# Kernel optimization log

Measured on AMD Instinct MI355X. Metric: run time of the kernel, lower is better.

The kernel has to match this reference:

```python
import jax, jax.numpy as jnp
import numpy as np
import math

DIM = 256

def setup_inputs() -> dict:
    key = jax.random.key(0)
    kx, kq, kk, kv = jax.random.split(key, 4)
    B, N, D = 2, 8192, DIM
    x = jax.random.normal(kx, (B, N, D), dtype=jnp.float32)
    s = 1.0 / math.sqrt(D)  # ~ PyTorch Linear init scale
    Wq = jax.random.uniform(kq, (D, D), dtype=jnp.float32, minval=-s, maxval=s)
    Wk = jax.random.uniform(kk, (D, D), dtype=jnp.float32, minval=-s, maxval=s)
    Wv = jax.random.uniform(kv, (D, D), dtype=jnp.float32, minval=-s, maxval=s)
    return {"x": x, "Wq": Wq, "Wk": Wk, "Wv": Wv}

def reference(x, Wq, Wk, Wv):
    # x: [B, N, D]; torch Linear computes x @ W.T
    Q = jnp.einsum('bnd,ed->bne', x, Wq)
    K = jnp.einsum('bnd,ed->bne', x, Wk)
    V = jnp.einsum('bnd,ed->bne', x, Wv)
    D = x.shape[-1]
    scores = jnp.einsum('bqd,bkd->bqk', Q, K) / jnp.sqrt(jnp.float32(D))
    # NOTE: softmax over dim=1 (the query axis), matching the original code
    attn = jax.nn.softmax(scores, axis=1)  # [B, N, N]
    out = jnp.einsum('bqk,bkd->bqd', attn, V)
    return out
```

## Files before the change

### kernel.cpp

```cpp
#include <hip/hip_runtime.h>
#include <hip/hip_bf16.h>


#define N_ 8192
#define SCALE 0.0625f

typedef __attribute__((ext_vector_type(8))) short short8;
typedef __attribute__((ext_vector_type(4))) float f32x4;
typedef __attribute__((ext_vector_type(4))) unsigned short ushort4_t;

__device__ inline unsigned short f2bf(float f) {
    unsigned int x = __float_as_uint(f);
    unsigned int r = (x + 0x7fffu + ((x >> 16) & 1u)) >> 16;
    return (unsigned short)r;
}

__device__ inline short8 ldg8(const unsigned short* p) {
    return *reinterpret_cast<const short8*>(p);
}

__device__ inline short8 cvt8(const float* p) {
    float4 a = *(const float4*)p;
    float4 b = *(const float4*)(p + 4);
    short8 r;
    r[0] = (short)f2bf(a.x); r[1] = (short)f2bf(a.y);
    r[2] = (short)f2bf(a.z); r[3] = (short)f2bf(a.w);
    r[4] = (short)f2bf(b.x); r[5] = (short)f2bf(b.y);
    r[6] = (short)f2bf(b.z); r[7] = (short)f2bf(b.w);
    return r;
}

__device__ inline f32x4 mfma16(short8 a, short8 b, f32x4 c) {
    return __builtin_amdgcn_mfma_f32_16x16x32_bf16(a, b, c, 0, 0, 0);
}

__device__ inline float bf2f(unsigned short u) {
    return __uint_as_float(((unsigned)u) << 16);
}

#define PIN8(v) asm volatile("" : "+v"(v))

typedef __attribute__((address_space(3))) unsigned int lds_u32;
typedef __attribute__((address_space(1))) const unsigned int glb_u32;
__device__ __forceinline__ void gll16(const void* g, void* l) {
    __builtin_amdgcn_global_load_lds((glb_u32*)g, (lds_u32*)l, 16, 0, 0);
}
#define WAIT_VM0()   asm volatile("s_waitcnt vmcnt(0)" ::: "memory")
#define WAIT_LGKM0() asm volatile("s_waitcnt lgkmcnt(0)" ::: "memory")
#define BARRIER()    __builtin_amdgcn_s_barrier()

__global__ __launch_bounds__(256) void k_cvtw(
    const float* __restrict__ Wq, const float* __restrict__ Wk,
    const float* __restrict__ Wv, unsigned short* __restrict__ Wb)
{
    int t = blockIdx.x * 256 + threadIdx.x;
    int e8 = t * 8;
    const float* src = (e8 < 65536) ? Wq + e8
                     : (e8 < 131072) ? Wk + (e8 - 65536)
                                     : Wv + (e8 - 131072);
    *reinterpret_cast<short8*>(Wb + e8) = cvt8(src);
}

__global__ __launch_bounds__(512, 1) void k_proj(
    const float* __restrict__ x, const unsigned short* __restrict__ Wb,
    unsigned short* __restrict__ Qb, unsigned short* __restrict__ Kb,
    unsigned short* __restrict__ Vt)
{
    extern __shared__ char smem[];
    unsigned short* sX = (unsigned short*)smem;
    char* sW = smem + 32768;
    const int rb = blockIdx.x;
    const int tid = threadIdx.x, w = tid >> 6, lane = tid & 63;
    const int lr = lane & 15, lg = lane >> 4;
    const int wqs = w >> 2, wes = w & 3;

    int eoff[4], doff[4];
#pragma unroll
    for (int i = 0; i < 4; ++i) {
        int L = tid + i * 512;
        int r = L >> 5, c = (L & 31) ^ (r & 7);
        eoff[i] = r * 256 + c * 8;
        doff[i] = L * 16;
    }

    const unsigned short* wsrc = Wb;
#pragma unroll
    for (int i = 0; i < 4; ++i)
        gll16(wsrc + eoff[i], sW + doff[i]);

#pragma unroll
    for (int i = 0; i < 4; ++i) {
        int g = tid + i * 512;
        int r = g >> 5, c = g & 31;
        int off = (r * 512 + c * 16) ^ ((r & 7) << 4);
        *reinterpret_cast<short8*>(reinterpret_cast<char*>(sX) + off) =
            cvt8(x + (size_t)(rb * 64 + r) * 256 + c * 8);
    }
    __syncthreads();

    short8 xf[2][8];
#pragma unroll
    for (int qf = 0; qf < 2; ++qf)
#pragma unroll
        for (int ks = 0; ks < 8; ++ks) {
            int row = wqs * 32 + qf * 16 + lr;
            int off = (row * 512 + (ks * 32 + lg * 8) * 2) ^ ((row & 7) << 4);
            xf[qf][ks] = *reinterpret_cast<const short8*>(
                reinterpret_cast<const char*>(sX) + off);
            PIN8(xf[qf][ks]);
        }

    for (int c = 0; c < 12; ++c) {
        const int cur = c & 1;
        const char* sWc = sW + cur * 32768;

        WAIT_VM0();
        BARRIER();
        __builtin_amdgcn_sched_barrier(0);

        if (c + 1 < 12) {
            const unsigned short* wn = Wb + (size_t)(c + 1) * 64 * 256;
            char* nW = sW + (cur ^ 1) * 32768;
#pragma unroll
            for (int i = 0; i < 4; ++i)
                gll16(wn + eoff[i], nW + doff[i]);
        }

        f32x4 acc[2] = {};
#pragma unroll
        for (int ks = 0; ks < 8; ++ks) {
            int row = wes * 16 + lr;
            int off = (row * 512 + (ks * 32 + lg * 8) * 2) ^ ((row & 7) << 4);
            short8 wf = *reinterpret_cast<const short8*>(sWc + off);
            acc[0] = mfma16(xf[0][ks], wf, acc[0]);
            acc[1] = mfma16(xf[1][ks], wf, acc[1]);
        }

        int mat = c >> 2;
        int ecol = (c & 3) * 64 + wes * 16 + lr;
#pragma unroll
        for (int qf = 0; qf < 2; ++qf) {
            int rbase = rb * 64 + wqs * 32 + qf * 16 + lg * 4;
            if (mat < 2) {
                unsigned short* dst = (mat == 0) ? Qb : Kb;
#pragma unroll
                for (int r = 0; r < 4; ++r)
                    dst[(size_t)(rbase + r) * 256 + ecol] = f2bf(acc[qf][r]);
            } else {
                int bidx = rbase >> 13, nr = rbase & 8191;
                ushort4_t v;
#pragma unroll
                for (int r = 0; r < 4; ++r) v[r] = f2bf(acc[qf][r]);
                *reinterpret_cast<ushort4_t*>(
                    Vt + ((size_t)bidx * 256 + ecol) * 8192 + nr) = v;
            }
        }
    }
}

__global__ __launch_bounds__(512, 1) void k_zv(
    const unsigned short* __restrict__ Qb, const unsigned short* __restrict__ Kb,
    unsigned short* __restrict__ Vt)
{
    extern __shared__ char smem[];
    __shared__ float zred[8][32];
    __shared__ float zfin[64];
    const int kt = blockIdx.x, b = blockIdx.y;
    const int tid = threadIdx.x, w = tid >> 6, lane = tid & 63;
    const int lr = lane & 15, lg = lane >> 4;
    const int qs = w & 3, kh = w >> 2;

    short8 kfr[2][8];
#pragma unroll
    for (int kn = 0; kn < 2; ++kn)
#pragma unroll
        for (int ks = 0; ks < 8; ++ks) {
            kfr[kn][ks] = ldg8(
                Kb + (size_t)(b * N_ + kt * 64 + kh * 32 + kn * 16 + lr) * 256
                   + ks * 32 + lg * 8);
            PIN8(kfr[kn][ks]);
        }

    int eoff[8], doff[8];
#pragma unroll
    for (int i = 0; i < 8; ++i) {
        int L = i * 512 + w * 64 + lane;
        int r = L >> 5, c = (L & 31) ^ (r & 7);
        eoff[i] = r * 256 + c * 8;
        doff[i] = L * 16;
    }
    const unsigned short* qbase = Qb + (size_t)b * N_ * 256;

#pragma unroll
    for (int i = 0; i < 8; ++i)
        gll16(qbase + eoff[i], smem + doff[i]);

    float zs0 = 0.f, zs1 = 0.f;
    for (int it = 0; it < 64; ++it) {
        const int cur = it & 1;
        const char* sQ = smem + cur * 65536;

        WAIT_VM0();
        BARRIER();
        __builtin_amdgcn_sched_barrier(0);

        if (it + 1 < 64) {
            const unsigned short* qsrc = qbase + (size_t)(it + 1) * 128 * 256;
            char* nQ = smem + (cur ^ 1) * 65536;
#pragma unroll
            for (int i = 0; i < 8; ++i)
                gll16(qsrc + eoff[i], nQ + doff[i]);
        }

        f32x4 acc[2][2] = {};
        __builtin_amdgcn_s_setprio(1);
#pragma unroll
        for (int ks = 0; ks < 8; ++ks) {
            int coff = (ks * 32 + lg * 8) * 2;
#pragma unroll
            for (int qf = 0; qf < 2; ++qf) {
                int row = qs * 32 + qf * 16 + lr;
                int off = (row * 512 + coff) ^ ((row & 7) << 4);
                short8 qa = *reinterpret_cast<const short8*>(sQ + off);
                acc[qf][0] = mfma16(qa, kfr[0][ks], acc[qf][0]);
                acc[qf][1] = mfma16(qa, kfr[1][ks], acc[qf][1]);
            }
        }
        __builtin_amdgcn_s_setprio(0);

#pragma unroll
        for (int qf = 0; qf < 2; ++qf)
#pragma unroll
            for (int r = 0; r < 4; ++r) {
                zs0 += __expf(acc[qf][0][r] * SCALE);
                zs1 += __expf(acc[qf][1][r] * SCALE);
            }
    }

    zs0 += __shfl_xor(zs0, 16); zs0 += __shfl_xor(zs0, 32);
    zs1 += __shfl_xor(zs1, 16); zs1 += __shfl_xor(zs1, 32);
    if (lg == 0) {
        zred[w][lr]      = zs0;
        zred[w][16 + lr] = zs1;
    }
    __syncthreads();
    if (tid < 64) {
        int kh2 = tid >> 5, kc = tid & 31;
        float z = zred[kh2 * 4 + 0][kc] + zred[kh2 * 4 + 1][kc] +
                  zred[kh2 * 4 + 2][kc] + zred[kh2 * 4 + 3][kc];
        zfin[tid] = 1.0f / z;
    }
    __syncthreads();

#pragma unroll
    for (int i = 0; i < 4; ++i) {
        int G = i * 512 + tid;
        int d = G >> 3, c = G & 7;
        unsigned short* p =
            Vt + ((size_t)b * 256 + d) * 8192 + kt * 64 + c * 8;
        short8 v = *reinterpret_cast<short8*>(p);
        short8 o;
#pragma unroll
        for (int j = 0; j < 8; ++j)
            o[j] = (short)f2bf(bf2f((unsigned short)v[j]) * zfin[c * 8 + j]);
        *reinterpret_cast<short8*>(p) = o;
    }
}

__global__ __launch_bounds__(512, 1) void k_attn(
    const unsigned short* __restrict__ Qb, const unsigned short* __restrict__ Kb,
    const unsigned short* __restrict__ Vt, float* __restrict__ out)
{
    extern __shared__ char smem[];
    const int qt = blockIdx.x, b = blockIdx.y;
    const int tid = threadIdx.x, w = tid >> 6, lane = tid & 63;
    const int lr = lane & 15, lg = lane >> 4;
    const int qbase = qt * 64;
    const int wqs = w >> 2;
    const int wks = w & 3;
    const int wds = w & 3;
    const int q0 = wqs * 32;

    const unsigned short* srcK[4];
    const unsigned short* srcV[4];
#pragma unroll
    for (int i = 0; i < 4; ++i) {
        int L = w * 256 + i * 64 + lane;
        int r = L >> 5, c = (L & 31) ^ (r & 7);
        srcK[i] = Kb + (size_t)(b * N_ + r) * 256 + c * 8;
        int d = L >> 3, c2 = (L & 7) ^ (d & 7);
        srcV[i] = Vt + ((size_t)b * 256 + d) * 8192 + c2 * 8;
    }

#pragma unroll
    for (int i = 0; i < 4; ++i) {
        gll16(srcK[i], smem + (size_t)(w * 256 + i * 64) * 16);
        gll16(srcV[i], smem + 65536 + (size_t)(w * 256 + i * 64) * 16);
        srcK[i] += 64 * 256;
        srcV[i] += 64;
    }

    short8 qfr[2][8];
#pragma unroll
    for (int qf = 0; qf < 2; ++qf) {
        const unsigned short* qrow =
            Qb + (size_t)(b * N_ + qbase + q0 + qf * 16 + lr) * 256;
#pragma unroll
        for (int ks = 0; ks < 8; ++ks) {
            qfr[qf][ks] = ldg8(qrow + ks * 32 + lg * 8);
            PIN8(qfr[qf][ks]);
        }
    }

    f32x4 acco[2][4] = {};

    for (int kt = 0; kt < 128; ++kt) {
        const int cur = kt & 1;
        char* sK = smem + cur * 32768;
        char* sV = smem + 65536 + cur * 32768;
        char* sP = smem + 131072;

        WAIT_VM0();
        BARRIER();
        __builtin_amdgcn_sched_barrier(0);

        if (kt + 1 < 128) {
            char* nK = smem + (cur ^ 1) * 32768;
            char* nV = smem + 65536 + (cur ^ 1) * 32768;
#pragma unroll
            for (int i = 0; i < 4; ++i) {
                gll16(srcK[i], nK + (size_t)(w * 256 + i * 64) * 16);
                gll16(srcV[i], nV + (size_t)(w * 256 + i * 64) * 16);
                srcK[i] += 64 * 256;
                srcV[i] += 64;
            }
        }

        f32x4 sacc[2] = {};
        __builtin_amdgcn_s_setprio(1);
#pragma unroll
        for (int ks = 0; ks < 8; ++ks) {
            int krow = wks * 16 + lr;
            int coff = (ks * 32 + lg * 8) * 2;
            int off = (krow * 512 + coff) ^ ((krow & 7) << 4);
            short8 kb = *reinterpret_cast<const short8*>(sK + off);
            sacc[0] = mfma16(qfr[0][ks], kb, sacc[0]);
            sacc[1] = mfma16(qfr[1][ks], kb, sacc[1]);
        }
        __builtin_amdgcn_s_setprio(0);

#pragma unroll
        for (int qf = 0; qf < 2; ++qf)
#pragma unroll
            for (int r = 0; r < 4; ++r) {
                float p = __expf(sacc[qf][r] * SCALE);
                int q = q0 + qf * 16 + lg * 4 + r;
                int kcol = wks * 16 + lr;
                int off = (q * 128 + kcol * 2) ^ ((q & 7) << 4);
                *reinterpret_cast<unsigned short*>(sP + off) = f2bf(p);
            }

        WAIT_LGKM0();
        BARRIER();
        __builtin_amdgcn_sched_barrier(0);

        __builtin_amdgcn_s_setprio(1);
#pragma unroll
        for (int kk = 0; kk < 2; ++kk) {
            int coff = (kk * 32 + lg * 8) * 2;
            short8 pa[2];
#pragma unroll
            for (int qf = 0; qf < 2; ++qf) {
                int qq = q0 + qf * 16 + lr;
                int offa = (qq * 128 + coff) ^ ((qq & 7) << 4);
                pa[qf] = *reinterpret_cast<const short8*>(sP + offa);
            }
#pragma unroll
            for (int df = 0; df < 4; ++df) {
                int d = wds * 64 + df * 16 + lr;
                int offb = (d * 128 + coff) ^ ((d & 7) << 4);
                short8 vb = *reinterpret_cast<const short8*>(sV + offb);
                acco[0][df] = mfma16(pa[0], vb, acco[0][df]);
                acco[1][df] = mfma16(pa[1], vb, acco[1][df]);
            }
        }
        __builtin_amdgcn_s_setprio(0);
    }

#pragma unroll
    for (int qf = 0; qf < 2; ++qf)
#pragma unroll
        for (int df = 0; df < 4; ++df) {
            int d = wds * 64 + df * 16 + lr;
            int q0r = qbase + q0 + qf * 16 + lg * 4;
#pragma unroll
            for (int r = 0; r < 4; ++r)
                out[(size_t)(b * N_ + q0r + r) * 256 + d] = acco[qf][df][r];
        }
}

extern "C" void kernel_launch(void* const* d_in, const int* in_sizes, int n_in,
                              void* d_out, int out_size, void* d_ws, size_t ws_size,
                              hipStream_t stream)
{
    const float* x  = (const float*)d_in[0];
    const float* Wq = (const float*)d_in[1];
    const float* Wk = (const float*)d_in[2];
    const float* Wv = (const float*)d_in[3];

    char* ws = (char*)d_ws;
    unsigned short* Qb = (unsigned short*)(ws);
    unsigned short* Kb = (unsigned short*)(ws + 8388608);
    unsigned short* Vt = (unsigned short*)(ws + 16777216);
    unsigned short* Wb = (unsigned short*)(ws + 25165824);
    float* out = (float*)d_out;

    k_cvtw<<<dim3(96), dim3(256), 0, stream>>>(Wq, Wk, Wv, Wb);

    hipFuncSetAttribute((const void*)k_proj,
                        hipFuncAttributeMaxDynamicSharedMemorySize, 98304);
    k_proj<<<dim3(256), dim3(512), 98304, stream>>>(x, Wb, Qb, Kb, Vt);

    hipFuncSetAttribute((const void*)k_zv,
                        hipFuncAttributeMaxDynamicSharedMemorySize, 131072);
    k_zv<<<dim3(128, 2), dim3(512), 131072, stream>>>(Qb, Kb, Vt);

    hipFuncSetAttribute((const void*)k_attn,
                        hipFuncAttributeMaxDynamicSharedMemorySize, 139264);
    k_attn<<<dim3(128, 2), dim3(512), 139264, stream>>>(Qb, Kb, Vt, out);
}
```

Before: 300.8 us.

## Enlarge attention query tile to 128 and split key range across two blocks

Each attention block now covers 128 queries instead of 64, so every K/V tile loaded into shared memory serves twice as many queries. Each wave computes a 32-key by 32-query score tile and 128 output dims. To keep the grid at 256 blocks on the GPU, the key axis is split in two. The second half writes partial sums to a workspace buffer, and a new add kernel merges them into the output. This trades lower K/V traffic per query for more registers per wave, an extra fp32 partial write and read, and one more kernel launch.

```diff
diff --git a/kernel.cpp b/kernel.cpp
--- a/kernel.cpp
+++ b/kernel.cpp
@@ -269,17 +269,19 @@
 
 __global__ __launch_bounds__(512, 1) void k_attn(
     const unsigned short* __restrict__ Qb, const unsigned short* __restrict__ Kb,
-    const unsigned short* __restrict__ Vt, float* __restrict__ out)
+    const unsigned short* __restrict__ Vt, float* __restrict__ out,
+    float* __restrict__ part, int nkt)
 {
     extern __shared__ char smem[];
-    const int qt = blockIdx.x, b = blockIdx.y;
+    const int qt = blockIdx.x, kh = blockIdx.y, b = blockIdx.z;
     const int tid = threadIdx.x, w = tid >> 6, lane = tid & 63;
     const int lr = lane & 15, lg = lane >> 4;
-    const int qbase = qt * 64;
-    const int wqs = w >> 2;
-    const int wks = w & 3;
-    const int wds = w & 3;
+    const int qbase = qt * 128;
+    const int wqs = w >> 1;
+    const int wkh = w & 1;
+    const int wds = w & 1;
     const int q0 = wqs * 32;
+    const int k0 = kh * nkt * 64;
 
     const unsigned short* srcK[4];
     const unsigned short* srcV[4];
@@ -287,9 +289,9 @@
     for (int i = 0; i < 4; ++i) {
         int L = w * 256 + i * 64 + lane;
         int r = L >> 5, c = (L & 31) ^ (r & 7);
-        srcK[i] = Kb + (size_t)(b * N_ + r) * 256 + c * 8;
+        srcK[i] = Kb + (size_t)(b * N_ + k0 + r) * 256 + c * 8;
         int d = L >> 3, c2 = (L & 7) ^ (d & 7);
-        srcV[i] = Vt + ((size_t)b * 256 + d) * 8192 + c2 * 8;
+        srcV[i] = Vt + ((size_t)b * 256 + d) * 8192 + k0 + c2 * 8;
     }
 
 #pragma unroll
@@ -312,9 +314,9 @@
         }
     }
 
-    f32x4 acco[2][4] = {};
-
-    for (int kt = 0; kt < 128; ++kt) {
+    f32x4 acco[2][8] = {};
+
+    for (int kt = 0; kt < nkt; ++kt) {
         const int cur = kt & 1;
         char* sK = smem + cur * 32768;
         char* sV = smem + 65536 + cur * 32768;
@@ -324,7 +326,7 @@
         BARRIER();
         __builtin_amdgcn_sched_barrier(0);
 
-        if (kt + 1 < 128) {
+        if (kt + 1 < nkt) {
             char* nK = smem + (cur ^ 1) * 32768;
             char* nV = smem + 65536 + (cur ^ 1) * 32768;
 #pragma unroll
@@ -336,29 +338,34 @@
             }
         }
 
-        f32x4 sacc[2] = {};
+        f32x4 sacc[2][2] = {};
         __builtin_amdgcn_s_setprio(1);
 #pragma unroll
         for (int ks = 0; ks < 8; ++ks) {
-            int krow = wks * 16 + lr;
             int coff = (ks * 32 + lg * 8) * 2;
-            int off = (krow * 512 + coff) ^ ((krow & 7) << 4);
-            short8 kb = *reinterpret_cast<const short8*>(sK + off);
-            sacc[0] = mfma16(qfr[0][ks], kb, sacc[0]);
-            sacc[1] = mfma16(qfr[1][ks], kb, sacc[1]);
+#pragma unroll
+            for (int kf = 0; kf < 2; ++kf) {
+                int krow = wkh * 32 + kf * 16 + lr;
+                int off = (krow * 512 + coff) ^ ((krow & 7) << 4);
+                short8 kb = *reinterpret_cast<const short8*>(sK + off);
+                sacc[0][kf] = mfma16(qfr[0][ks], kb, sacc[0][kf]);
+                sacc[1][kf] = mfma16(qfr[1][ks], kb, sacc[1][kf]);
+            }
         }
         __builtin_amdgcn_s_setprio(0);
 
 #pragma unroll
         for (int qf = 0; qf < 2; ++qf)
 #pragma unroll
-            for (int r = 0; r < 4; ++r) {
-                float p = __expf(sacc[qf][r] * SCALE);
-                int q = q0 + qf * 16 + lg * 4 + r;
-                int kcol = wks * 16 + lr;
-                int off = (q * 128 + kcol * 2) ^ ((q & 7) << 4);
-                *reinterpret_cast<unsigned short*>(sP + off) = f2bf(p);
-            }
+            for (int kf = 0; kf < 2; ++kf)
+#pragma unroll
+                for (int r = 0; r < 4; ++r) {
+                    float p = __expf(sacc[qf][kf][r] * SCALE);
+                    int q = q0 + qf * 16 + lg * 4 + r;
+                    int kcol = wkh * 32 + kf * 16 + lr;
+                    int off = (q * 128 + kcol * 2) ^ ((q & 7) << 4);
+                    *reinterpret_cast<unsigned short*>(sP + off) = f2bf(p);
+                }
 
         WAIT_LGKM0();
         BARRIER();
@@ -376,8 +383,8 @@
                 pa[qf] = *reinterpret_cast<const short8*>(sP + offa);
             }
 #pragma unroll
-            for (int df = 0; df < 4; ++df) {
-                int d = wds * 64 + df * 16 + lr;
+            for (int df = 0; df < 8; ++df) {
+                int d = wds * 128 + df * 16 + lr;
                 int offb = (d * 128 + coff) ^ ((d & 7) << 4);
                 short8 vb = *reinterpret_cast<const short8*>(sV + offb);
                 acco[0][df] = mfma16(pa[0], vb, acco[0][df]);
@@ -387,16 +394,31 @@
         __builtin_amdgcn_s_setprio(0);
     }
 
+    float* dst = (kh == 0) ? out : part;
 #pragma unroll
     for (int qf = 0; qf < 2; ++qf)
 #pragma unroll
-        for (int df = 0; df < 4; ++df) {
-            int d = wds * 64 + df * 16 + lr;
+        for (int df = 0; df < 8; ++df) {
+            int d = wds * 128 + df * 16 + lr;
             int q0r = qbase + q0 + qf * 16 + lg * 4;
 #pragma unroll
             for (int r = 0; r < 4; ++r)
-                out[(size_t)(b * N_ + q0r + r) * 256 + d] = acco[qf][df][r];
-        }
+                dst[(size_t)(b * N_ + q0r + r) * 256 + d] = acco[qf][df][r];
+        }
+}
+
+__global__ __launch_bounds__(256) void k_add(
+    float* __restrict__ out, const float* __restrict__ part)
+{
+    int t = blockIdx.x * 256 + threadIdx.x;
+#pragma unroll
+    for (int i = 0; i < 4; ++i) {
+        int idx = t + i * 262144;
+        float4 a = reinterpret_cast<float4*>(out)[idx];
+        float4 p = reinterpret_cast<const float4*>(part)[idx];
+        a.x += p.x; a.y += p.y; a.z += p.z; a.w += p.w;
+        reinterpret_cast<float4*>(out)[idx] = a;
+    }
 }
 
 extern "C" void kernel_launch(void* const* d_in, const int* in_sizes, int n_in,
@@ -413,6 +435,7 @@
     unsigned short* Kb = (unsigned short*)(ws + 8388608);
     unsigned short* Vt = (unsigned short*)(ws + 16777216);
     unsigned short* Wb = (unsigned short*)(ws + 25165824);
+    float* part1       = (float*)(ws + 25559040);
     float* out = (float*)d_out;
 
     k_cvtw<<<dim3(96), dim3(256), 0, stream>>>(Wq, Wk, Wv, Wb);
@@ -426,6 +449,13 @@
     k_zv<<<dim3(128, 2), dim3(512), 131072, stream>>>(Qb, Kb, Vt);
 
     hipFuncSetAttribute((const void*)k_attn,
-                        hipFuncAttributeMaxDynamicSharedMemorySize, 139264);
-    k_attn<<<dim3(128, 2), dim3(512), 139264, stream>>>(Qb, Kb, Vt, out);
-}
+                        hipFuncAttributeMaxDynamicSharedMemorySize, 147456);
+    if (ws_size >= (size_t)25559040 + 16777216) {
+        k_attn<<<dim3(64, 2, 2), dim3(512), 147456, stream>>>(
+            Qb, Kb, Vt, out, part1, 64);
+        k_add<<<dim3(1024), dim3(256), 0, stream>>>(out, part1);
+    } else {
+        k_attn<<<dim3(64, 1, 2), dim3(512), 147456, stream>>>(
+            Qb, Kb, Vt, out, out, 128);
+    }
+}
```

New measurement: 252.3 us, median of 5. 1.19x faster.
